# Kernel tuning notes

Hardware: AMD Instinct MI355X
Metric: run time of the kernel (lower is better)

The kernel has to match this reference:

```python
import jax, jax.numpy as jnp
import numpy as np

B, S, H = 2, 2048, 1024
NUM_HEAD = 16
HEAD = H // NUM_HEAD
NEG = -10000000000.0


def setup_inputs() -> dict:
    key = jax.random.key(0)
    ks = jax.random.split(key, 10)
    scale = 1.0 / np.sqrt(H)
    return {
        "query": jax.random.normal(ks[0], (B, S, H), jnp.float32),
        "key": jax.random.normal(ks[1], (B, S, H), jnp.float32),
        "value": jax.random.normal(ks[2], (B, S, H), jnp.float32),
        "mask": jax.random.randint(ks[3], (B, S), 0, 2, jnp.int32),
        "Wq": jax.random.normal(ks[4], (H, H), jnp.float32) * scale,
        "bq": jnp.zeros((H,), jnp.float32),
        "Wk": jax.random.normal(ks[5], (H, H), jnp.float32) * scale,
        "bk": jnp.zeros((H,), jnp.float32),
        "Wv": jax.random.normal(ks[6], (H, H), jnp.float32) * scale,
        "bv": jnp.zeros((H,), jnp.float32),
    }


def reference(query, key, value, mask, Wq, bq, Wk, bk, Wv, bv):
    b, s, h = query.shape
    # Linear projections (torch Linear: x @ W.T + b), split into heads -> [b, nh, s, hd]
    def proj(x, W, bias):
        y = x @ W.T + bias
        return y.reshape(b, s, NUM_HEAD, HEAD).transpose(0, 2, 1, 3)

    q = proj(query, Wq, bq)
    k = proj(key, Wk, bk)
    v = proj(value, Wv, bv)

    # NOTE: original module has NO 1/sqrt(head_dim) scaling -- faithful.
    attn_score = jnp.einsum("bhqd,bhkd->bhqk", q, k)  # [b, nh, s, s]
    # key-padding mask bias: 0 where mask==1, -1e10 where mask==0, broadcast over query dim
    bias_add = jnp.where(mask[:, None, None, :] == 0, NEG, 0.0).astype(attn_score.dtype)
    attn_score = attn_score + bias_add
    attn_ratio = jax.nn.softmax(attn_score, axis=-1)
    out = jnp.einsum("bhqk,bhkd->bhqd", attn_ratio, v)  # [b, nh, s, hd]
    out = out.transpose(0, 2, 1, 3).reshape(b, s, h)
    # Dropout is identity in eval mode; output_linear is defined but never used in forward.
    return out
```

## Files before the change

### kernel.cpp

```cpp
#include <hip/hip_runtime.h>

#define BATCH 2
#define S_LEN 2048
#define HDIM  1024
#define NHEAD 16
#define HD    64
#define NEGBIAS -1e10f

typedef __attribute__((ext_vector_type(8))) _Float16 half8;
typedef __attribute__((ext_vector_type(4))) _Float16 half4;
typedef __attribute__((ext_vector_type(4))) float   f32x4;

__global__ __launch_bounds__(256) void proj_gemm_f16(
    const float* __restrict__ Xq, const float* __restrict__ Wq, const float* __restrict__ bq,
    const float* __restrict__ Xk, const float* __restrict__ Wk, const float* __restrict__ bk,
    const float* __restrict__ Xv, const float* __restrict__ Wv, const float* __restrict__ bv,
    _Float16* __restrict__ Qb, _Float16* __restrict__ Kb, _Float16* __restrict__ Vtb)
{
    const int z = blockIdx.z;
    const float* X    = (z == 0) ? Xq : (z == 1) ? Xk : Xv;
    const float* W    = (z == 0) ? Wq : (z == 1) ? Wk : Wv;
    const float* bias = (z == 0) ? bq : (z == 1) ? bk : bv;
    _Float16* Y       = (z == 0) ? Qb : (z == 1) ? Kb : Vtb;

    const int n0 = blockIdx.x * 128;
    const int m0 = blockIdx.y * 128;

    __shared__ __align__(16) _Float16 As[128][40];
    __shared__ __align__(16) _Float16 Bs[128][40];

    const int t    = threadIdx.x;
    const int w    = t >> 6;
    const int lane = t & 63;
    const int quad = lane >> 4;
    const int lc   = lane & 15;
    const int wm   = (w >> 1) * 64;
    const int wn   = (w & 1) * 64;

    const f32x4 fzero = {0.f, 0.f, 0.f, 0.f};
    f32x4 acc[4][4];
#pragma unroll
    for (int i = 0; i < 4; i++)
#pragma unroll
        for (int j = 0; j < 4; j++) acc[i][j] = fzero;

    const int srow = t >> 2;
    const int sc   = t & 3;

    float4 xa[2][2], wa[2][2];
#define PROJ_ISSUE(K0)                                                        \
    {                                                                         \
        _Pragma("unroll")                                                     \
        for (int hf = 0; hf < 2; hf++) {                                      \
            const float* gx = X + (size_t)(m0 + srow + hf * 64) * HDIM + (K0) + sc * 8; \
            xa[hf][0] = *(const float4*)gx;                                   \
            xa[hf][1] = *(const float4*)(gx + 4);                             \
            const float* gw = W + (size_t)(n0 + srow + hf * 64) * HDIM + (K0) + sc * 8; \
            wa[hf][0] = *(const float4*)gw;                                   \
            wa[hf][1] = *(const float4*)(gw + 4);                             \
        }                                                                     \
    }

    PROJ_ISSUE(0)

    for (int k0 = 0; k0 < HDIM; k0 += 32) {
        if (k0) __syncthreads();
#pragma unroll
        for (int hf = 0; hf < 2; hf++) {
            int row = srow + hf * 64;
            half8 vx;
            vx[0] = (_Float16)xa[hf][0].x; vx[1] = (_Float16)xa[hf][0].y;
            vx[2] = (_Float16)xa[hf][0].z; vx[3] = (_Float16)xa[hf][0].w;
            vx[4] = (_Float16)xa[hf][1].x; vx[5] = (_Float16)xa[hf][1].y;
            vx[6] = (_Float16)xa[hf][1].z; vx[7] = (_Float16)xa[hf][1].w;
            *(half8*)&As[row][sc * 8] = vx;
            half8 vw;
            vw[0] = (_Float16)wa[hf][0].x; vw[1] = (_Float16)wa[hf][0].y;
            vw[2] = (_Float16)wa[hf][0].z; vw[3] = (_Float16)wa[hf][0].w;
            vw[4] = (_Float16)wa[hf][1].x; vw[5] = (_Float16)wa[hf][1].y;
            vw[6] = (_Float16)wa[hf][1].z; vw[7] = (_Float16)wa[hf][1].w;
            *(half8*)&Bs[row][sc * 8] = vw;
        }
        __syncthreads();

        if (k0 + 32 < HDIM) PROJ_ISSUE(k0 + 32)

        half8 af[4], bf[4];
#pragma unroll
        for (int mt = 0; mt < 4; mt++)
            af[mt] = *(const half8*)&As[wm + mt * 16 + lc][quad * 8];
#pragma unroll
        for (int nt = 0; nt < 4; nt++)
            bf[nt] = *(const half8*)&Bs[wn + nt * 16 + lc][quad * 8];
#pragma unroll
        for (int mt = 0; mt < 4; mt++)
#pragma unroll
            for (int nt = 0; nt < 4; nt++)
                acc[mt][nt] = __builtin_amdgcn_mfma_f32_16x16x32_f16(
                    af[mt], bf[nt], acc[mt][nt], 0, 0, 0);
    }

#pragma unroll
    for (int nt = 0; nt < 4; nt++) {
        const int n = n0 + wn + nt * 16 + lc;
        const float bv_ = bias[n];
        const int h = n >> 6, d = n & 63;
#pragma unroll
        for (int mt = 0; mt < 4; mt++) {
#pragma unroll
            for (int r = 0; r < 4; r++) {
                const int m = m0 + wm + mt * 16 + quad * 4 + r;
                const int b = m >> 11, s = m & (S_LEN - 1);
                const int bh = b * NHEAD + h;
                _Float16 val = (_Float16)(acc[mt][nt][r] + bv_);
                if (z == 2)
                    Y[((size_t)bh * HD + d) * S_LEN + s] = val;
                else
                    Y[((size_t)bh * S_LEN + s) * HD + d] = val;
            }
        }
    }
}

__global__ __launch_bounds__(256) void flash_attn_mfma(
    const _Float16* __restrict__ Qb, const _Float16* __restrict__ Kb,
    const _Float16* __restrict__ Vtb, const int* __restrict__ mask,
    float* __restrict__ out)
{
    const int qt = blockIdx.x & 15;
    const int bh = blockIdx.x >> 4;
    const int b  = bh >> 4;
    const int h  = bh & (NHEAD - 1);

    __shared__ __align__(16) _Float16 Ks [64][72];
    __shared__ __align__(16) _Float16 Vts[64][72];
    __shared__ __align__(16) _Float16 Ps [4][32][72];
    __shared__ float biasS[64];

    const int t    = threadIdx.x;
    const int w    = t >> 6;
    const int lane = t & 63;
    const int quad = lane >> 4;
    const int lc   = lane & 15;

    const _Float16* Kbase = Kb  + (size_t)bh * S_LEN * HD;
    const _Float16* Vbase = Vtb + (size_t)bh * HD * S_LEN;
    const int* mbase = mask + b * S_LEN;

    half8 qf[2][2];
#pragma unroll
    for (int qg = 0; qg < 2; qg++) {
        const int qrow = qt * 128 + w * 32 + qg * 16 + lc;
#pragma unroll
        for (int s = 0; s < 2; s++)
            qf[qg][s] = *(const half8*)(Qb + ((size_t)bh * S_LEN + qrow) * HD
                                        + s * 32 + quad * 8);
    }

    const f32x4 fzero = {0.f, 0.f, 0.f, 0.f};
    f32x4 o[2][4];
#pragma unroll
    for (int qg = 0; qg < 2; qg++)
#pragma unroll
        for (int nt = 0; nt < 4; nt++) o[qg][nt] = fzero;
    float mrun[2] = {-3.0e38f, -3.0e38f};
    float lrun[2] = {0.f, 0.f};

    const int rr0 = t >> 3,          cc0 = (t & 7) * 8;
    const int rr1 = (t + 256) >> 3,  cc1 = (t & 7) * 8;

    half8 kpre[2], vpre[2];
    int   mpre;
#define ATTN_ISSUE(KT)                                                        \
    {                                                                         \
        kpre[0] = *(const half8*)(Kbase + (size_t)((KT) + rr0) * HD + cc0);   \
        kpre[1] = *(const half8*)(Kbase + (size_t)((KT) + rr1) * HD + cc1);   \
        vpre[0] = *(const half8*)(Vbase + (size_t)rr0 * S_LEN + (KT) + cc0);  \
        vpre[1] = *(const half8*)(Vbase + (size_t)rr1 * S_LEN + (KT) + cc1);  \
        mpre    = mbase[(KT) + (t & 63)];                                     \
    }

    ATTN_ISSUE(0)

    for (int kt = 0; kt < S_LEN; kt += 64) {
        if (kt) __syncthreads();
        *(half8*)&Ks [rr0][cc0] = kpre[0];
        *(half8*)&Ks [rr1][cc1] = kpre[1];
        *(half8*)&Vts[rr0][cc0] = vpre[0];
        *(half8*)&Vts[rr1][cc1] = vpre[1];
        if (t < 64) biasS[t] = mpre ? 0.f : NEGBIAS;
        __syncthreads();

        if (kt + 64 < S_LEN) ATTN_ISSUE(kt + 64)

        f32x4 scf[2][4];
#pragma unroll
        for (int qg = 0; qg < 2; qg++)
#pragma unroll
            for (int tt = 0; tt < 4; tt++) scf[qg][tt] = fzero;
#pragma unroll
        for (int s = 0; s < 2; s++) {
#pragma unroll
            for (int tt = 0; tt < 4; tt++) {
                half8 kf = *(const half8*)&Ks[tt * 16 + lc][s * 32 + quad * 8];
                scf[0][tt] = __builtin_amdgcn_mfma_f32_16x16x32_f16(kf, qf[0][s], scf[0][tt], 0, 0, 0);
                scf[1][tt] = __builtin_amdgcn_mfma_f32_16x16x32_f16(kf, qf[1][s], scf[1][tt], 0, 0, 0);
            }
        }

#pragma unroll
        for (int tt = 0; tt < 4; tt++) {
            float4 b4 = *(const float4*)&biasS[tt * 16 + quad * 4];
#pragma unroll
            for (int qg = 0; qg < 2; qg++) {
                scf[qg][tt][0] += b4.x; scf[qg][tt][1] += b4.y;
                scf[qg][tt][2] += b4.z; scf[qg][tt][3] += b4.w;
            }
        }

#pragma unroll
        for (int qg = 0; qg < 2; qg++) {
            float mx = scf[qg][0][0];
#pragma unroll
            for (int tt = 0; tt < 4; tt++)
#pragma unroll
                for (int r = 0; r < 4; r++) mx = fmaxf(mx, scf[qg][tt][r]);
            mx = fmaxf(mx, __shfl_xor(mx, 16));
            mx = fmaxf(mx, __shfl_xor(mx, 32));

            float mn = fmaxf(mrun[qg], mx);
            float al = __expf(mrun[qg] - mn);
            float ls = 0.f;
#pragma unroll
            for (int tt = 0; tt < 4; tt++)
#pragma unroll
                for (int r = 0; r < 4; r++) {
                    float p = __expf(scf[qg][tt][r] - mn);
                    scf[qg][tt][r] = p;
                    ls += p;
                }
            ls += __shfl_xor(ls, 16);
            ls += __shfl_xor(ls, 32);
            lrun[qg] = lrun[qg] * al + ls;
            mrun[qg] = mn;
#pragma unroll
            for (int nt = 0; nt < 4; nt++) {
                o[qg][nt][0] *= al; o[qg][nt][1] *= al;
                o[qg][nt][2] *= al; o[qg][nt][3] *= al;
            }

#pragma unroll
            for (int tt = 0; tt < 4; tt++) {
                half4 pk;
                pk[0] = (_Float16)scf[qg][tt][0]; pk[1] = (_Float16)scf[qg][tt][1];
                pk[2] = (_Float16)scf[qg][tt][2]; pk[3] = (_Float16)scf[qg][tt][3];
                *(half4*)&Ps[w][qg * 16 + lc][tt * 16 + quad * 4] = pk;
            }
        }

#pragma unroll
        for (int s = 0; s < 2; s++) {
            half8 pf0 = *(const half8*)&Ps[w][lc]     [s * 32 + quad * 8];
            half8 pf1 = *(const half8*)&Ps[w][16 + lc][s * 32 + quad * 8];
#pragma unroll
            for (int nt = 0; nt < 4; nt++) {
                half8 vf = *(const half8*)&Vts[nt * 16 + lc][s * 32 + quad * 8];
                o[0][nt] = __builtin_amdgcn_mfma_f32_16x16x32_f16(vf, pf0, o[0][nt], 0, 0, 0);
                o[1][nt] = __builtin_amdgcn_mfma_f32_16x16x32_f16(vf, pf1, o[1][nt], 0, 0, 0);
            }
        }
    }

#pragma unroll
    for (int qg = 0; qg < 2; qg++) {
        const int qrow = qt * 128 + w * 32 + qg * 16 + lc;
        const float inv = 1.f / lrun[qg];
        const size_t rowb = ((size_t)b * S_LEN + qrow) * HDIM + h * HD;
#pragma unroll
        for (int nt = 0; nt < 4; nt++) {
            float4 v;
            v.x = o[qg][nt][0] * inv; v.y = o[qg][nt][1] * inv;
            v.z = o[qg][nt][2] * inv; v.w = o[qg][nt][3] * inv;
            *(float4*)&out[rowb + nt * 16 + quad * 4] = v;
        }
    }
}

extern "C" void kernel_launch(void* const* d_in, const int* in_sizes, int n_in,
                              void* d_out, int out_size, void* d_ws, size_t ws_size,
                              hipStream_t stream) {
    const float* query = (const float*)d_in[0];
    const float* key   = (const float*)d_in[1];
    const float* value = (const float*)d_in[2];
    const int*   mask  = (const int*)  d_in[3];
    const float* Wq    = (const float*)d_in[4];
    const float* bq    = (const float*)d_in[5];
    const float* Wk    = (const float*)d_in[6];
    const float* bk    = (const float*)d_in[7];
    const float* Wv    = (const float*)d_in[8];
    const float* bv    = (const float*)d_in[9];
    float* out = (float*)d_out;

    const size_t nElem = (size_t)BATCH * S_LEN * HDIM;
    if (ws_size < 3 * nElem * sizeof(_Float16)) return;
    _Float16* Qb  = (_Float16*)d_ws;
    _Float16* Kb  = Qb + nElem;
    _Float16* Vtb = Kb + nElem;

    dim3 gproj(HDIM / 128, (BATCH * S_LEN) / 128, 3);
    proj_gemm_f16<<<gproj, 256, 0, stream>>>(query, Wq, bq, key, Wk, bk,
                                             value, Wv, bv, Qb, Kb, Vtb);

    flash_attn_mfma<<<BATCH * NHEAD * (S_LEN / 128), 256, 0, stream>>>(
        Qb, Kb, Vtb, mask, out);
}
```

Before: 243.9 us.

## Halve attention query tile, fold log2e into Q, lazy rescale, swizzle blocks

Each attention block now handles 64 query rows instead of 128, one 16-row group per wave, which doubles the grid to 1024 blocks and cuts per-thread registers; launch bounds request 4 blocks per CU. The Q projection pre-multiplies by log2(e) so softmax can use exp2f. The running-max rescale of the accumulators is skipped while every lane's new max stays within 8 of the running max. Probabilities are packed with cvt_pkrtz, and block IDs are swizzled across heads and query tiles. The trade-off is that K/V tiles are loaded twice as often overall, since each tile now serves fewer query rows.

```diff
diff --git a/kernel.cpp b/kernel.cpp
--- a/kernel.cpp
+++ b/kernel.cpp
@@ -6,6 +6,7 @@
 #define NHEAD 16
 #define HD    64
 #define NEGBIAS -1e10f
+#define LOG2E 1.44269504088896f
 
 typedef __attribute__((ext_vector_type(8))) _Float16 half8;
 typedef __attribute__((ext_vector_type(4))) _Float16 half4;
@@ -112,7 +113,9 @@
                 const int m = m0 + wm + mt * 16 + quad * 4 + r;
                 const int b = m >> 11, s = m & (S_LEN - 1);
                 const int bh = b * NHEAD + h;
-                _Float16 val = (_Float16)(acc[mt][nt][r] + bv_);
+                float y = acc[mt][nt][r] + bv_;
+                if (z == 0) y *= LOG2E;
+                _Float16 val = (_Float16)y;
                 if (z == 2)
                     Y[((size_t)bh * HD + d) * S_LEN + s] = val;
                 else
@@ -122,19 +125,21 @@
     }
 }
 
-__global__ __launch_bounds__(256) void flash_attn_mfma(
+__global__ __launch_bounds__(256, 4) void flash_attn_mfma(
     const _Float16* __restrict__ Qb, const _Float16* __restrict__ Kb,
     const _Float16* __restrict__ Vtb, const int* __restrict__ mask,
     float* __restrict__ out)
 {
-    const int qt = blockIdx.x & 15;
-    const int bh = blockIdx.x >> 4;
+    const int bid = blockIdx.x;
+    const int swz = (bid & 7) * 128 + (bid >> 3);
+    const int qt = swz & 31;
+    const int bh = swz >> 5;
     const int b  = bh >> 4;
     const int h  = bh & (NHEAD - 1);
 
     __shared__ __align__(16) _Float16 Ks [64][72];
     __shared__ __align__(16) _Float16 Vts[64][72];
-    __shared__ __align__(16) _Float16 Ps [4][32][72];
+    __shared__ __align__(16) _Float16 Ps [4][16][72];
     __shared__ float biasS[64];
 
     const int t    = threadIdx.x;
@@ -147,24 +152,19 @@
     const _Float16* Vbase = Vtb + (size_t)bh * HD * S_LEN;
     const int* mbase = mask + b * S_LEN;
 
-    half8 qf[2][2];
-#pragma unroll
-    for (int qg = 0; qg < 2; qg++) {
-        const int qrow = qt * 128 + w * 32 + qg * 16 + lc;
-#pragma unroll
-        for (int s = 0; s < 2; s++)
-            qf[qg][s] = *(const half8*)(Qb + ((size_t)bh * S_LEN + qrow) * HD
-                                        + s * 32 + quad * 8);
-    }
+    const int qrow = qt * 64 + w * 16 + lc;
+    half8 qf[2];
+#pragma unroll
+    for (int s = 0; s < 2; s++)
+        qf[s] = *(const half8*)(Qb + ((size_t)bh * S_LEN + qrow) * HD
+                                + s * 32 + quad * 8);
 
     const f32x4 fzero = {0.f, 0.f, 0.f, 0.f};
-    f32x4 o[2][4];
-#pragma unroll
-    for (int qg = 0; qg < 2; qg++)
-#pragma unroll
-        for (int nt = 0; nt < 4; nt++) o[qg][nt] = fzero;
-    float mrun[2] = {-3.0e38f, -3.0e38f};
-    float lrun[2] = {0.f, 0.f};
+    f32x4 o[4];
+#pragma unroll
+    for (int nt = 0; nt < 4; nt++) o[nt] = fzero;
+    float mrun = -3.0e38f;
+    float lrun = 0.f;
 
     const int rr0 = t >> 3,          cc0 = (t & 7) * 8;
     const int rr1 = (t + 256) >> 3,  cc1 = (t & 7) * 8;
@@ -193,96 +193,85 @@
 
         if (kt + 64 < S_LEN) ATTN_ISSUE(kt + 64)
 
-        f32x4 scf[2][4];
-#pragma unroll
-        for (int qg = 0; qg < 2; qg++)
-#pragma unroll
-            for (int tt = 0; tt < 4; tt++) scf[qg][tt] = fzero;
+        f32x4 scf[4];
+#pragma unroll
+        for (int tt = 0; tt < 4; tt++) scf[tt] = fzero;
 #pragma unroll
         for (int s = 0; s < 2; s++) {
 #pragma unroll
             for (int tt = 0; tt < 4; tt++) {
                 half8 kf = *(const half8*)&Ks[tt * 16 + lc][s * 32 + quad * 8];
-                scf[0][tt] = __builtin_amdgcn_mfma_f32_16x16x32_f16(kf, qf[0][s], scf[0][tt], 0, 0, 0);
-                scf[1][tt] = __builtin_amdgcn_mfma_f32_16x16x32_f16(kf, qf[1][s], scf[1][tt], 0, 0, 0);
+                scf[tt] = __builtin_amdgcn_mfma_f32_16x16x32_f16(kf, qf[s], scf[tt], 0, 0, 0);
             }
         }
 
 #pragma unroll
         for (int tt = 0; tt < 4; tt++) {
             float4 b4 = *(const float4*)&biasS[tt * 16 + quad * 4];
-#pragma unroll
-            for (int qg = 0; qg < 2; qg++) {
-                scf[qg][tt][0] += b4.x; scf[qg][tt][1] += b4.y;
-                scf[qg][tt][2] += b4.z; scf[qg][tt][3] += b4.w;
-            }
-        }
-
-#pragma unroll
-        for (int qg = 0; qg < 2; qg++) {
-            float mx = scf[qg][0][0];
-#pragma unroll
-            for (int tt = 0; tt < 4; tt++)
-#pragma unroll
-                for (int r = 0; r < 4; r++) mx = fmaxf(mx, scf[qg][tt][r]);
-            mx = fmaxf(mx, __shfl_xor(mx, 16));
-            mx = fmaxf(mx, __shfl_xor(mx, 32));
-
-            float mn = fmaxf(mrun[qg], mx);
-            float al = __expf(mrun[qg] - mn);
-            float ls = 0.f;
-#pragma unroll
-            for (int tt = 0; tt < 4; tt++)
-#pragma unroll
-                for (int r = 0; r < 4; r++) {
-                    float p = __expf(scf[qg][tt][r] - mn);
-                    scf[qg][tt][r] = p;
-                    ls += p;
-                }
-            ls += __shfl_xor(ls, 16);
-            ls += __shfl_xor(ls, 32);
-            lrun[qg] = lrun[qg] * al + ls;
-            mrun[qg] = mn;
+            scf[tt][0] += b4.x; scf[tt][1] += b4.y;
+            scf[tt][2] += b4.z; scf[tt][3] += b4.w;
+        }
+
+        float mx = scf[0][0];
+#pragma unroll
+        for (int tt = 0; tt < 4; tt++)
+#pragma unroll
+            for (int r = 0; r < 4; r++) mx = fmaxf(mx, scf[tt][r]);
+        mx = fmaxf(mx, __shfl_xor(mx, 16));
+        mx = fmaxf(mx, __shfl_xor(mx, 32));
+
+        if (!__all(mx <= mrun + 8.f)) {
+            float mn = fmaxf(mrun, mx);
+            float al = exp2f(mrun - mn);
+            lrun *= al;
 #pragma unroll
             for (int nt = 0; nt < 4; nt++) {
-                o[qg][nt][0] *= al; o[qg][nt][1] *= al;
-                o[qg][nt][2] *= al; o[qg][nt][3] *= al;
-            }
-
-#pragma unroll
-            for (int tt = 0; tt < 4; tt++) {
-                half4 pk;
-                pk[0] = (_Float16)scf[qg][tt][0]; pk[1] = (_Float16)scf[qg][tt][1];
-                pk[2] = (_Float16)scf[qg][tt][2]; pk[3] = (_Float16)scf[qg][tt][3];
-                *(half4*)&Ps[w][qg * 16 + lc][tt * 16 + quad * 4] = pk;
-            }
+                o[nt][0] *= al; o[nt][1] *= al;
+                o[nt][2] *= al; o[nt][3] *= al;
+            }
+            mrun = mn;
+        }
+
+        float ls = 0.f;
+#pragma unroll
+        for (int tt = 0; tt < 4; tt++)
+#pragma unroll
+            for (int r = 0; r < 4; r++) {
+                float p = exp2f(scf[tt][r] - mrun);
+                scf[tt][r] = p;
+                ls += p;
+            }
+        ls += __shfl_xor(ls, 16);
+        ls += __shfl_xor(ls, 32);
+        lrun += ls;
+
+#pragma unroll
+        for (int tt = 0; tt < 4; tt++) {
+            auto pk01 = __builtin_amdgcn_cvt_pkrtz(scf[tt][0], scf[tt][1]);
+            auto pk23 = __builtin_amdgcn_cvt_pkrtz(scf[tt][2], scf[tt][3]);
+            auto pk   = __builtin_shufflevector(pk01, pk23, 0, 1, 2, 3);
+            *(decltype(pk)*)&Ps[w][lc][tt * 16 + quad * 4] = pk;
         }
 
 #pragma unroll
         for (int s = 0; s < 2; s++) {
-            half8 pf0 = *(const half8*)&Ps[w][lc]     [s * 32 + quad * 8];
-            half8 pf1 = *(const half8*)&Ps[w][16 + lc][s * 32 + quad * 8];
+            half8 pf = *(const half8*)&Ps[w][lc][s * 32 + quad * 8];
 #pragma unroll
             for (int nt = 0; nt < 4; nt++) {
                 half8 vf = *(const half8*)&Vts[nt * 16 + lc][s * 32 + quad * 8];
-                o[0][nt] = __builtin_amdgcn_mfma_f32_16x16x32_f16(vf, pf0, o[0][nt], 0, 0, 0);
-                o[1][nt] = __builtin_amdgcn_mfma_f32_16x16x32_f16(vf, pf1, o[1][nt], 0, 0, 0);
-            }
-        }
-    }
-
-#pragma unroll
-    for (int qg = 0; qg < 2; qg++) {
-        const int qrow = qt * 128 + w * 32 + qg * 16 + lc;
-        const float inv = 1.f / lrun[qg];
-        const size_t rowb = ((size_t)b * S_LEN + qrow) * HDIM + h * HD;
-#pragma unroll
-        for (int nt = 0; nt < 4; nt++) {
-            float4 v;
-            v.x = o[qg][nt][0] * inv; v.y = o[qg][nt][1] * inv;
-            v.z = o[qg][nt][2] * inv; v.w = o[qg][nt][3] * inv;
-            *(float4*)&out[rowb + nt * 16 + quad * 4] = v;
-        }
+                o[nt] = __builtin_amdgcn_mfma_f32_16x16x32_f16(vf, pf, o[nt], 0, 0, 0);
+            }
+        }
+    }
+
+    const float inv = 1.f / lrun;
+    const size_t rowb = ((size_t)b * S_LEN + qrow) * HDIM + h * HD;
+#pragma unroll
+    for (int nt = 0; nt < 4; nt++) {
+        float4 v;
+        v.x = o[nt][0] * inv; v.y = o[nt][1] * inv;
+        v.z = o[nt][2] * inv; v.w = o[nt][3] * inv;
+        *(float4*)&out[rowb + nt * 16 + quad * 4] = v;
     }
 }
 
@@ -311,6 +300,6 @@
     proj_gemm_f16<<<gproj, 256, 0, stream>>>(query, Wq, bq, key, Wk, bk,
                                              value, Wv, bv, Qb, Kb, Vtb);
 
-    flash_attn_mfma<<<BATCH * NHEAD * (S_LEN / 128), 256, 0, stream>>>(
+    flash_attn_mfma<<<BATCH * NHEAD * (S_LEN / 64), 256, 0, stream>>>(
         Qb, Kb, Vtb, mask, out);
 }
```

Result: no change. 247.6 us (+1.5%).
